# Kernel tuning notes

Measured on AMD Instinct MI355X. Metric: run time of the kernel, lower is better.

Reference implementation:

```python
import jax, jax.numpy as jnp
import numpy as np

N = 100000
D = 512   # input_size
C = 2     # output_class
QDIM = 128


def setup_inputs() -> dict:
    key = jax.random.key(0)
    ks = jax.random.split(key, 12)
    s = 0.02
    return {
        "feats": jax.random.normal(ks[0], (N, D), jnp.float32),
        "c": jax.random.normal(ks[1], (N, C), jnp.float32),
        "single_predictions": jax.random.normal(ks[2], (N, 1), jnp.float32),
        # self.lin = Linear(D, D) + ReLU
        "W_lin": jax.random.normal(ks[3], (D, D), jnp.float32) * s,
        "b_lin": jnp.zeros((D,), jnp.float32),
        # self.q = Linear(D, 128) + Tanh
        "W_q": jax.random.normal(ks[4], (QDIM, D), jnp.float32) * s,
        "b_q": jnp.zeros((QDIM,), jnp.float32),
        # self.v = Dropout(0.0) + Linear(D, D)
        "W_v": jax.random.normal(ks[5], (D, D), jnp.float32) * s,
        "b_v": jnp.zeros((D,), jnp.float32),
        # self.fcc = Conv1d(C, C, kernel_size=D)
        "W_fcc": jax.random.normal(ks[6], (C, C, D), jnp.float32) * s,
        "b_fcc": jnp.zeros((C,), jnp.float32),
    }


def reference(feats, c, single_predictions, W_lin, b_lin, W_q, b_q, W_v, b_v, W_fcc, b_fcc):
    n = feats.shape[0]
    k = int(0.2 * n)

    preds = single_predictions[:, 0]                      # [N]
    # torch.topk(largest=False): indices of the k smallest; zero them out
    _, lastk_idx = jax.lax.top_k(-preds, k)
    preds = preds.at[lastk_idx].set(0.0)
    instance_score = jax.nn.softmax(preds, axis=0)[:, None]  # [N,1], softmax over instances

    f = feats * instance_score + feats                    # [N,D]
    f = jax.nn.relu(f @ W_lin.T + b_lin)                  # self.lin
    V = f @ W_v.T + b_v                                   # [N,D] (dropout p=0)
    Q = jnp.tanh(f @ W_q.T + b_q)                         # [N,128]

    # torch.sort(c, 0, descending)[1][0,:] == per-class argmax over instances
    m_indices = jnp.argmax(c, axis=0)                     # [C]
    m_feats = f[m_indices]                                # [C,D]
    q_max = jnp.tanh(m_feats @ W_q.T + b_q)               # [C,128]

    A = Q @ q_max.T                                       # [N,C]
    A = jax.nn.softmax(A / jnp.sqrt(jnp.float32(QDIM)), axis=0)  # softmax over instances
    B = A.T @ V                                           # [C,D]

    # Conv1d(C, C, kernel=D) on B[None] -> length-1 output: full contraction
    Cout = jnp.einsum('id,oid->o', B, W_fcc) + b_fcc      # [C]
    return Cout[None, :], A, B
```

## Files before the change

kernel.cpp:

```cpp
#include <hip/hip_runtime.h>
#include <stdint.h>

typedef unsigned short u16;
typedef __bf16 bf16t;
typedef bf16t bf16x8 __attribute__((ext_vector_type(8)));
typedef float f32x4 __attribute__((ext_vector_type(4)));
typedef unsigned long long ull;

#define NROWS 100000
#define DD 512
#define QD 128
#define KSEL 20000
#define NB 1563

__device__ __forceinline__ uint32_t fmono(float x){
  uint32_t u = __float_as_uint(x);
  return (u & 0x80000000u) ? ~u : (u | 0x80000000u);
}
__device__ __forceinline__ float finv(uint32_t k){
  uint32_t u = (k & 0x80000000u) ? (k & 0x7fffffffu) : ~k;
  return __uint_as_float(u);
}
__device__ __forceinline__ u16 f2bf(float x){
  uint32_t u = __float_as_uint(x);
  u += 0x7fffu + ((u >> 16) & 1u);
  return (u16)(u >> 16);
}
__device__ __forceinline__ uint32_t pkbf(float a, float b){
  return (uint32_t)f2bf(a) | ((uint32_t)f2bf(b) << 16);
}

struct Scal {
  uint32_t keyT;
  float Z;
  uint32_t pad[14];
};

#define MFMA16(A,B,C) __builtin_amdgcn_mfma_f32_16x16x32_bf16(A,B,C,0,0,0)

__global__ void k_conv(const float* __restrict__ Wl, const float* __restrict__ Wv,
                       const float* __restrict__ Wq, u16* __restrict__ wl_bf, u16* __restrict__ wvq_bf,
                       uint32_t* __restrict__ hist, ull* __restrict__ cmax){
  int idx = blockIdx.x*256 + threadIdx.x;
  if (idx < 65536) hist[idx] = 0u;
  if (idx == 0){ cmax[0] = 0ull; cmax[1] = 0ull; }
  if (idx < 262144) wl_bf[idx] = f2bf(Wl[idx]);
  int e = idx - 262144;
  if (e >= 0) wvq_bf[e] = f2bf(e < 262144 ? Wv[e] : Wq[e - 262144]);
}

__global__ void k_sel1(const float* __restrict__ preds, const float* __restrict__ c,
                       uint32_t* __restrict__ hist, ull* __restrict__ cmax){
  __shared__ ull kr0[4], kr1[4];
  const int t = threadIdx.x;
  const int gid = blockIdx.x*256 + t;
  const int lane = t & 63;

  const float4* p4 = (const float4*)preds;
  for (int i = gid; i < 25000; i += 65536){
    float4 v = p4[i];
    atomicAdd(&hist[fmono(v.x) >> 16], 1u);
    atomicAdd(&hist[fmono(v.y) >> 16], 1u);
    atomicAdd(&hist[fmono(v.z) >> 16], 1u);
    atomicAdd(&hist[fmono(v.w) >> 16], 1u);
  }

  ull k0 = 0ull, k1 = 0ull;
  const float4* c4 = (const float4*)c;
  for (int i = gid; i < 50000; i += 65536){
    float4 v = c4[i];
    uint32_t r0 = 2u*i, r1 = 2u*i + 1u;
    ull a0 = ((ull)fmono(v.x) << 32) | (ull)(~r0);
    ull a1 = ((ull)fmono(v.z) << 32) | (ull)(~r1);
    ull b0 = ((ull)fmono(v.y) << 32) | (ull)(~r0);
    ull b1 = ((ull)fmono(v.w) << 32) | (ull)(~r1);
    if (a0 > k0) k0 = a0;
    if (a1 > k0) k0 = a1;
    if (b0 > k1) k1 = b0;
    if (b1 > k1) k1 = b1;
  }
  #pragma unroll
  for (int off = 32; off; off >>= 1){
    ull o0 = __shfl_xor(k0, off); if (o0 > k0) k0 = o0;
    ull o1 = __shfl_xor(k1, off); if (o1 > k1) k1 = o1;
  }
  if (lane == 0){ kr0[t >> 6] = k0; kr1[t >> 6] = k1; }
  __syncthreads();
  if (t == 0){
    ull m0 = kr0[0], m1 = kr1[0];
    #pragma unroll
    for (int w = 1; w < 4; ++w){
      if (kr0[w] > m0) m0 = kr0[w];
      if (kr1[w] > m1) m1 = kr1[w];
    }
    atomicMax(&cmax[0], m0);
    atomicMax(&cmax[1], m1);
  }
}

#define CAND_CAP 8192
__launch_bounds__(1024)
__global__ void k_prep2(const float* __restrict__ preds, const float* __restrict__ feats,
                        const float* __restrict__ Wl, const float* __restrict__ bl,
                        const float* __restrict__ Wq, const float* __restrict__ bq,
                        const uint32_t* __restrict__ hist, const ull* __restrict__ cmax,
                        Scal* __restrict__ sc, float* __restrict__ qmv){
  __shared__ uint32_t cand[CAND_CAP];
  __shared__ uint32_t wsum[16], woff[16];
  __shared__ float zred[16];
  __shared__ uint32_t s_B, s_cumBelow, s_keyT, candN;
  __shared__ float s_Z;
  __shared__ uint32_t s_mi[2];
  __shared__ float fmX[2][512];
  __shared__ float fmF[2][512];
  const int t = threadIdx.x;
  const int lane = t & 63, wv = t >> 6;

  if (t == 0){
    candN = 0;
    s_mi[0] = ~(uint32_t)(cmax[0] & 0xffffffffull);
    s_mi[1] = ~(uint32_t)(cmax[1] & 0xffffffffull);
  }

  const int b0 = t*64;
  uint32_t local = 0;
  {
    const uint4* h4 = (const uint4*)(hist + b0);
    #pragma unroll 4
    for (int q = 0; q < 16; ++q){ uint4 hv = h4[q]; local += hv.x + hv.y + hv.z + hv.w; }
  }
  uint32_t x = local;
  #pragma unroll
  for (int off = 1; off < 64; off <<= 1){
    uint32_t y = __shfl_up(x, off);
    if (lane >= off) x += y;
  }
  if (lane == 63) wsum[wv] = x;
  __syncthreads();
  if (t == 0){
    uint32_t cum = 0;
    for (int w = 0; w < 16; ++w){ woff[w] = cum; cum += wsum[w]; }
  }
  __syncthreads();
  uint32_t excl = x - local + woff[wv];
  if (excl < KSEL && excl + local >= KSEL){
    uint32_t cum = excl;
    for (int b = 0; b < 64; ++b){
      uint32_t h = hist[b0 + b];
      if (cum + h >= KSEL){ s_B = (uint32_t)(b0 + b); s_cumBelow = cum; break; }
      cum += h;
    }
  }
  __syncthreads();
  const uint32_t B = s_B;

  float sA = 0.f;
  const float4* p4 = (const float4*)preds;
  for (int i = t; i < 25000; i += 1024){
    float4 v = p4[i];
    float vv[4] = {v.x, v.y, v.z, v.w};
    #pragma unroll
    for (int e = 0; e < 4; ++e){
      uint32_t k = fmono(vv[e]);
      uint32_t bb = k >> 16;
      if (bb > B){
        sA += __expf(vv[e]);
      } else if (bb == B){
        uint32_t idx = atomicAdd(&candN, 1u);
        if (idx < CAND_CAP) cand[idx] = k;
      }
    }
  }
  #pragma unroll
  for (int off = 32; off; off >>= 1) sA += __shfl_xor(sA, off);
  if (lane == 0) zred[wv] = sA;
  __syncthreads();

  const uint32_t n = candN < CAND_CAP ? candN : CAND_CAP;
  const uint32_t r = KSEL - s_cumBelow;
  for (uint32_t i = t; i < n; i += 1024){
    uint32_t ki = cand[i];
    uint32_t less = 0, eq = 0;
    for (uint32_t j = 0; j < n; ++j){
      uint32_t kj = cand[j];
      less += (kj < ki) ? 1u : 0u;
      eq   += (kj == ki) ? 1u : 0u;
    }
    if (less < r && r <= less + eq) s_keyT = ki;
  }
  __syncthreads();
  const uint32_t keyT = s_keyT;

  float sCA = 0.f;
  for (uint32_t i = t; i < n; i += 1024){
    uint32_t k = cand[i];
    if (k > keyT) sCA += __expf(finv(k));
  }
  #pragma unroll
  for (int off = 32; off; off >>= 1) sCA += __shfl_xor(sCA, off);
  if (lane == 0) zred[wv] += sCA;
  __syncthreads();
  if (t == 0){
    float Z = (float)KSEL;
    for (int w = 0; w < 16; ++w) Z += zred[w];
    s_Z = Z;
    sc->keyT = keyT; sc->Z = Z;
  }
  __syncthreads();

  {
    int j = t >> 9, col = t & 511;
    fmX[j][col] = feats[(size_t)s_mi[j]*DD + col];
  }
  __syncthreads();

  {
    int nn = t >> 1, h = t & 1;
    const float4* wr4 = (const float4*)(Wl + (size_t)nn*DD + h*256);
    const float4* x04 = (const float4*)(&fmX[0][h*256]);
    const float4* x14 = (const float4*)(&fmX[1][h*256]);
    float a0 = 0.f, a1 = 0.f;
    #pragma unroll 4
    for (int k = 0; k < 64; ++k){
      float4 w = wr4[k], u = x04[k], v = x14[k];
      a0 += u.x*w.x + u.y*w.y + u.z*w.z + u.w*w.w;
      a1 += v.x*w.x + v.y*w.y + v.z*w.z + v.w*w.w;
    }
    a0 += __shfl_xor(a0, 1);
    a1 += __shfl_xor(a1, 1);
    if (h == 0){
      float Z = s_Z;
      float p0 = preds[s_mi[0]]; float q0 = (fmono(p0) <= keyT) ? 0.f : p0;
      float g0 = 1.f + __expf(q0) / Z;
      float p1 = preds[s_mi[1]]; float q1 = (fmono(p1) <= keyT) ? 0.f : p1;
      float g1 = 1.f + __expf(q1) / Z;
      float v0 = bl[nn] + g0*a0; fmF[0][nn] = v0 > 0.f ? v0 : 0.f;
      float v1 = bl[nn] + g1*a1; fmF[1][nn] = v1 > 0.f ? v1 : 0.f;
    }
  }
  __syncthreads();

  if (t < 256){
    int q = t & 127, j = t >> 7;
    const float4* wr4 = (const float4*)(Wq + (size_t)q*DD);
    const float4* x4  = (const float4*)(fmF[j]);
    float a0 = 0.f, a1 = 0.f;
    #pragma unroll 4
    for (int k = 0; k < 128; k += 2){
      float4 w0 = wr4[k], u0 = x4[k];
      float4 w1 = wr4[k+1], u1 = x4[k+1];
      a0 += u0.x*w0.x + u0.y*w0.y + u0.z*w0.z + u0.w*w0.w;
      a1 += u1.x*w1.x + u1.y*w1.y + u1.z*w1.z + u1.w*w1.w;
    }
    qmv[j*QD + q] = tanhf(bq[q] + a0 + a1);
  }
}

__device__ __forceinline__ const u16* chunk_src(const u16* __restrict__ wl,
                                                const u16* __restrict__ wvq,
                                                int ci, int r, int p){
  if (ci < 64){
    int nt = ci >> 4, kc = ci & 15;
    return wl + (size_t)(nt*128 + r)*DD + kc*32 + p*16;
  }
  int c2 = ci - 64;
  int nt2 = c2 >> 4, kc = c2 & 15;
  int colbase = (nt2 == 0) ? 512 : (nt2 - 1)*128;
  return wvq + (size_t)(colbase + r)*DD + kc*32 + p*16;
}

__launch_bounds__(256, 2)
__global__ void k_fused(const float* __restrict__ feats, const float* __restrict__ preds,
                        const u16* __restrict__ wl, const u16* __restrict__ wvq,
                        const float* __restrict__ bl, const float* __restrict__ bv,
                        const float* __restrict__ bq, const float* __restrict__ qmv,
                        const Scal* __restrict__ sc,
                        float* __restrict__ gpart, float* __restrict__ gpartE,
                        float* __restrict__ Aout){
  __shared__ __align__(16) u16 lds[38400];
  __shared__ __align__(16) float Ef[128];
  u16* AF = lds;
  u16* Wb = lds + 33280;
  float* sred = (float*)(lds + 33280);
  const int tid = threadIdx.x;
  const int lane = tid & 63, quad = lane >> 4, l16 = lane & 15;
  const int wave = tid >> 6, wm = wave >> 1, wn = wave & 1;
  const long i0 = (long)blockIdx.x * 64;
  const uint32_t keyT = sc->keyT;
  const float Z = sc->Z;

  {
    int row = lane;
    long ir = i0 + row; if (ir >= NROWS) ir = NROWS - 1;
    float p = preds[ir];
    float pm = (fmono(p) <= keyT) ? 0.f : p;
    float g = 1.f + __expf(pm) / Z;
    const float4* src = (const float4*)(feats + ir*DD + wave*128);
    u16* dst = AF + row*520 + wave*128;
    #pragma unroll
    for (int j = 0; j < 16; ++j){
      float4 a = src[2*j], b = src[2*j + 1];
      uint4 pk;
      pk.x = pkbf(a.x*g, a.y*g); pk.y = pkbf(a.z*g, a.w*g);
      pk.z = pkbf(b.x*g, b.y*g); pk.w = pkbf(b.z*g, b.w*g);
      *(uint4*)(dst + j*8) = pk;
    }
  }

  const int rS = tid >> 1, pS = tid & 1;
  u16* wdst = Wb + rS*40 + pS*16;
  uint4 w0, w1;
  { const u16* sp = chunk_src(wl, wvq, 0, rS, pS); w0 = *(const uint4*)sp; w1 = *(const uint4*)(sp + 8); }

  f32x4 acc[2][4];
  uint32_t pkF[4][16];
  int ci = 0;

  for (int nt = 0; nt < 4; ++nt){
    #pragma unroll
    for (int mi = 0; mi < 2; ++mi)
      #pragma unroll
      for (int ni = 0; ni < 4; ++ni) acc[mi][ni] = (f32x4){0.f,0.f,0.f,0.f};
    for (int kc = 0; kc < 16; ++kc, ++ci){
      __syncthreads();
      *(uint4*)wdst = w0; *(uint4*)(wdst + 8) = w1;
      __syncthreads();
      if (ci < 143){
        const u16* sp = chunk_src(wl, wvq, ci + 1, rS, pS);
        w0 = *(const uint4*)sp; w1 = *(const uint4*)(sp + 8);
      }
      bf16x8 a0 = *(const bf16x8*)&AF[(wm*32 + l16)*520 + kc*32 + quad*8];
      bf16x8 a1 = *(const bf16x8*)&AF[(wm*32 + 16 + l16)*520 + kc*32 + quad*8];
      bf16x8 b0 = *(const bf16x8*)&Wb[(wn*64 +  0 + l16)*40 + quad*8];
      bf16x8 b1 = *(const bf16x8*)&Wb[(wn*64 + 16 + l16)*40 + quad*8];
      bf16x8 b2 = *(const bf16x8*)&Wb[(wn*64 + 32 + l16)*40 + quad*8];
      bf16x8 b3 = *(const bf16x8*)&Wb[(wn*64 + 48 + l16)*40 + quad*8];
      acc[0][0] = MFMA16(a0, b0, acc[0][0]);
      acc[0][1] = MFMA16(a0, b1, acc[0][1]);
      acc[0][2] = MFMA16(a0, b2, acc[0][2]);
      acc[0][3] = MFMA16(a0, b3, acc[0][3]);
      acc[1][0] = MFMA16(a1, b0, acc[1][0]);
      acc[1][1] = MFMA16(a1, b1, acc[1][1]);
      acc[1][2] = MFMA16(a1, b2, acc[1][2]);
      acc[1][3] = MFMA16(a1, b3, acc[1][3]);
    }
    #pragma unroll
    for (int ni = 0; ni < 4; ++ni){
      float bb = bl[nt*128 + wn*64 + ni*16 + l16];
      #pragma unroll
      for (int mi = 0; mi < 2; ++mi){
        float e0 = acc[mi][ni][0] + bb; e0 = e0 > 0.f ? e0 : 0.f;
        float e1 = acc[mi][ni][1] + bb; e1 = e1 > 0.f ? e1 : 0.f;
        float e2 = acc[mi][ni][2] + bb; e2 = e2 > 0.f ? e2 : 0.f;
        float e3 = acc[mi][ni][3] + bb; e3 = e3 > 0.f ? e3 : 0.f;
        pkF[nt][mi*8 + ni*2 + 0] = pkbf(e0, e1);
        pkF[nt][mi*8 + ni*2 + 1] = pkbf(e2, e3);
      }
    }
  }

  __syncthreads();
  #pragma unroll
  for (int nt = 0; nt < 4; ++nt)
    #pragma unroll
    for (int ni = 0; ni < 4; ++ni)
      #pragma unroll
      for (int mi = 0; mi < 2; ++mi){
        int col = nt*128 + wn*64 + ni*16 + l16;
        int r0 = (wm*32 + mi*16 + quad*4)*520 + col;
        uint32_t x = pkF[nt][mi*8 + ni*2], y = pkF[nt][mi*8 + ni*2 + 1];
        AF[r0]        = (u16)x;
        AF[r0 + 520]  = (u16)(x >> 16);
        AF[r0 + 1040] = (u16)y;
        AF[r0 + 1560] = (u16)(y >> 16);
      }

  for (int nt2 = 0; nt2 < 5; ++nt2){
    #pragma unroll
    for (int mi = 0; mi < 2; ++mi)
      #pragma unroll
      for (int ni = 0; ni < 4; ++ni) acc[mi][ni] = (f32x4){0.f,0.f,0.f,0.f};
    for (int kc = 0; kc < 16; ++kc, ++ci){
      __syncthreads();
      *(uint4*)wdst = w0; *(uint4*)(wdst + 8) = w1;
      __syncthreads();
      if (ci < 143){
        const u16* sp = chunk_src(wl, wvq, ci + 1, rS, pS);
        w0 = *(const uint4*)sp; w1 = *(const uint4*)(sp + 8);
      }
      bf16x8 a0 = *(const bf16x8*)&AF[(wm*32 + l16)*520 + kc*32 + quad*8];
      bf16x8 a1 = *(const bf16x8*)&AF[(wm*32 + 16 + l16)*520 + kc*32 + quad*8];
      bf16x8 b0 = *(const bf16x8*)&Wb[(wn*64 +  0 + l16)*40 + quad*8];
      bf16x8 b1 = *(const bf16x8*)&Wb[(wn*64 + 16 + l16)*40 + quad*8];
      bf16x8 b2 = *(const bf16x8*)&Wb[(wn*64 + 32 + l16)*40 + quad*8];
      bf16x8 b3 = *(const bf16x8*)&Wb[(wn*64 + 48 + l16)*40 + quad*8];
      acc[0][0] = MFMA16(a0, b0, acc[0][0]);
      acc[0][1] = MFMA16(a0, b1, acc[0][1]);
      acc[0][2] = MFMA16(a0, b2, acc[0][2]);
      acc[0][3] = MFMA16(a0, b3, acc[0][3]);
      acc[1][0] = MFMA16(a1, b0, acc[1][0]);
      acc[1][1] = MFMA16(a1, b1, acc[1][1]);
      acc[1][2] = MFMA16(a1, b2, acc[1][2]);
      acc[1][3] = MFMA16(a1, b3, acc[1][3]);
    }
    if (nt2 == 0){
      float p0[2][4], p1[2][4];
      #pragma unroll
      for (int mi = 0; mi < 2; ++mi)
        #pragma unroll
        for (int e = 0; e < 4; ++e){ p0[mi][e] = 0.f; p1[mi][e] = 0.f; }
      #pragma unroll
      for (int ni = 0; ni < 4; ++ni){
        int qc = wn*64 + ni*16 + l16;
        float bqv = bq[qc], q0 = qmv[qc], q1 = qmv[QD + qc];
        #pragma unroll
        for (int mi = 0; mi < 2; ++mi)
          #pragma unroll
          for (int e = 0; e < 4; ++e){
            float tq = tanhf(acc[mi][ni][e] + bqv);
            p0[mi][e] += tq * q0;
            p1[mi][e] += tq * q1;
          }
      }
      #pragma unroll
      for (int off = 1; off <= 8; off <<= 1)
        #pragma unroll
        for (int mi = 0; mi < 2; ++mi)
          #pragma unroll
          for (int e = 0; e < 4; ++e){
            p0[mi][e] += __shfl_xor(p0[mi][e], off);
            p1[mi][e] += __shfl_xor(p1[mi][e], off);
          }
      __syncthreads();
      if (l16 == 0){
        #pragma unroll
        for (int mi = 0; mi < 2; ++mi)
          #pragma unroll
          for (int e = 0; e < 4; ++e){
            int row = wm*32 + mi*16 + quad*4 + e;
            sred[(row*2 + 0)*2 + wn] = p0[mi][e];
            sred[(row*2 + 1)*2 + wn] = p1[mi][e];
          }
      }
      __syncthreads();
      if (tid < 128){
        int row = tid >> 1, j = tid & 1;
        float sv = (sred[(row*2 + j)*2 + 0] + sred[(row*2 + j)*2 + 1]) * 0.08838834764831845f;
        bool valid = (i0 + row) < NROWS;
        float ev = valid ? __expf(sv) : 0.f;
        Ef[row*2 + j] = ev;
        if (valid) Aout[(i0 + row)*2 + j] = ev;
        float t2 = ev;
        #pragma unroll
        for (int off = 2; off <= 32; off <<= 1) t2 += __shfl_xor(t2, off);
        if (lane < 2) gpartE[(size_t)blockIdx.x*4 + (tid >> 6)*2 + j] = t2;
      }
      __syncthreads();
    } else {
      float e0[2][4], e1[2][4];
      #pragma unroll
      for (int mi = 0; mi < 2; ++mi)
        #pragma unroll
        for (int e = 0; e < 4; ++e){
          int row = wm*32 + mi*16 + quad*4 + e;
          e0[mi][e] = Ef[row*2 + 0];
          e1[mi][e] = Ef[row*2 + 1];
        }
      #pragma unroll
      for (int ni = 0; ni < 4; ++ni){
        int colv = (nt2 - 1)*128 + wn*64 + ni*16 + l16;
        float bvv = bv[colv];
        float b0 = 0.f, b1 = 0.f;
        #pragma unroll
        for (int mi = 0; mi < 2; ++mi)
          #pragma unroll
          for (int e = 0; e < 4; ++e){
            float v = acc[mi][ni][e] + bvv;
            b0 += v * e0[mi][e];
            b1 += v * e1[mi][e];
          }
        b0 += __shfl_xor(b0, 16); b0 += __shfl_xor(b0, 32);
        b1 += __shfl_xor(b1, 16); b1 += __shfl_xor(b1, 32);
        if (quad == 0){
          gpart[((size_t)blockIdx.x*2 + wm)*1024 + colv]       = b0;
          gpart[((size_t)blockIdx.x*2 + wm)*1024 + 512 + colv] = b1;
        }
      }
    }
  }
}

__global__ void k_red(const float* __restrict__ gpart, const float* __restrict__ gpartE,
                      float* __restrict__ sumEV, float* __restrict__ sumE){
  const int t = threadIdx.x;
  if (blockIdx.x == 256){
    __shared__ float r0[256], r1[256];
    float s0 = 0.f, s1 = 0.f;
    for (int i = t; i < NB*2; i += 256){ s0 += gpartE[(size_t)i*2]; s1 += gpartE[(size_t)i*2 + 1]; }
    r0[t] = s0; r1[t] = s1;
    __syncthreads();
    for (int st = 128; st; st >>= 1){
      if (t < st){ r0[t] += r0[t + st]; r1[t] += r1[t + st]; }
      __syncthreads();
    }
    if (t == 0){ sumE[0] = r0[0]; sumE[1] = r1[0]; }
    return;
  }
  __shared__ float4 red[256];
  int col4 = blockIdx.x * 4;
  float4 s = {0.f, 0.f, 0.f, 0.f};
  for (int r = t; r < NB*2; r += 256){
    float4 v = *(const float4*)(gpart + (size_t)r*1024 + col4);
    s.x += v.x; s.y += v.y; s.z += v.z; s.w += v.w;
  }
  red[t] = s;
  __syncthreads();
  for (int st = 128; st; st >>= 1){
    if (t < st){
      float4 o = red[t + st];
      red[t].x += o.x; red[t].y += o.y; red[t].z += o.z; red[t].w += o.w;
    }
    __syncthreads();
  }
  if (t == 0) *(float4*)(sumEV + col4) = red[0];
}

__global__ void k_post(float* __restrict__ out, const float* __restrict__ sumE,
                       const float* __restrict__ sumEV, const float* __restrict__ Wfcc,
                       const float* __restrict__ bfcc){
  if (blockIdx.x < 782){
    int idx = blockIdx.x*256 + threadIdx.x;
    if (idx < 200000) out[2 + idx] = out[2 + idx] / sumE[idx & 1];
    return;
  }
  __shared__ float red[512];
  int t = threadIdx.x;
  float z0 = sumE[0], z1 = sumE[1];
  float c0 = 0.f, c1 = 0.f;
  for (int e = t; e < 1024; e += 256){
    float bvv = sumEV[e] / ((e >> 9) ? z1 : z0);
    out[200002 + e] = bvv;
    c0 += bvv * Wfcc[e];
    c1 += bvv * Wfcc[1024 + e];
  }
  red[t] = c0; red[256 + t] = c1;
  __syncthreads();
  for (int s = 128; s; s >>= 1){
    if (t < s){ red[t] += red[t + s]; red[256 + t] += red[256 + t + s]; }
    __syncthreads();
  }
  if (t == 0){ out[0] = red[0] + bfcc[0]; out[1] = red[256] + bfcc[1]; }
}

extern "C" void kernel_launch(void* const* d_in, const int* in_sizes, int n_in,
                              void* d_out, int out_size, void* d_ws, size_t ws_size,
                              hipStream_t stream){
  (void)in_sizes; (void)n_in; (void)out_size; (void)ws_size;
  const float* feats = (const float*)d_in[0];
  const float* c     = (const float*)d_in[1];
  const float* preds = (const float*)d_in[2];
  const float* W_lin = (const float*)d_in[3];
  const float* b_lin = (const float*)d_in[4];
  const float* W_q   = (const float*)d_in[5];
  const float* b_q   = (const float*)d_in[6];
  const float* W_v   = (const float*)d_in[7];
  const float* b_v   = (const float*)d_in[8];
  const float* W_fcc = (const float*)d_in[9];
  const float* b_fcc = (const float*)d_in[10];
  float* out = (float*)d_out;
  char* ws = (char*)d_ws;

  u16*   wl_bf  = (u16*)(ws + 0);
  u16*   wvq_bf = (u16*)(ws + 524288);
  Scal*  sc     = (Scal*)(ws + 1179648);
  float* qmv    = (float*)(ws + 1179712);
  float* sumE   = (float*)(ws + 1180736);
  float* sumEV  = (float*)(ws + 1180800);
  float* gpartE = (float*)(ws + 1184896);
  float* gpart  = (float*)(ws + 1209984);
  uint32_t* hist = (uint32_t*)(ws + 1209984);
  ull*      cmax = (ull*)(ws + 1209984 + 262144);

  k_conv <<<2304, 256, 0, stream>>>(W_lin, W_v, W_q, wl_bf, wvq_bf, hist, cmax);
  k_sel1 <<<256, 256, 0, stream>>>(preds, c, hist, cmax);
  k_prep2<<<1, 1024, 0, stream>>>(preds, feats, W_lin, b_lin, W_q, b_q, hist, cmax, sc, qmv);
  k_fused<<<NB, 256, 0, stream>>>(feats, preds, wl_bf, wvq_bf, b_lin, b_v, b_q,
                                  qmv, sc, gpart, gpartE, out + 2);
  k_red  <<<257, 256, 0, stream>>>(gpart, gpartE, sumEV, sumE);
  k_post <<<783, 256, 0, stream>>>(out, sumE, sumEV, W_fcc, b_fcc);
}
```

Baseline: 732.3 us.

## Double-buffer weight chunks in LDS with XOR swizzle and pre-tiled weight layout

The weight conversion kernel now writes bf16 weights already tiled into contiguous 128x32 chunks in the order the fused kernel consumes them, so each thread does one contiguous 32-byte load per chunk. The fused kernel switches from a single LDS weight buffer with two barriers per k-step to ping-pong buffers with one barrier per step and a two-chunk-deep register prefetch. Padded LDS rows are replaced by XOR-swizzled layouts to avoid bank conflicts. The exp weights are also kept in registers instead of an LDS array. The intent is to hide global load latency and halve barrier cost in the MFMA loop, at the price of more complex indexing and extra registers.

```diff
diff --git a/kernel.cpp b/kernel.cpp
--- a/kernel.cpp
+++ b/kernel.cpp
@@ -39,14 +39,26 @@
 #define MFMA16(A,B,C) __builtin_amdgcn_mfma_f32_16x16x32_bf16(A,B,C,0,0,0)
 
 __global__ void k_conv(const float* __restrict__ Wl, const float* __restrict__ Wv,
-                       const float* __restrict__ Wq, u16* __restrict__ wl_bf, u16* __restrict__ wvq_bf,
+                       const float* __restrict__ Wq, u16* __restrict__ wch,
                        uint32_t* __restrict__ hist, ull* __restrict__ cmax){
   int idx = blockIdx.x*256 + threadIdx.x;
   if (idx < 65536) hist[idx] = 0u;
   if (idx == 0){ cmax[0] = 0ull; cmax[1] = 0ull; }
-  if (idx < 262144) wl_bf[idx] = f2bf(Wl[idx]);
-  int e = idx - 262144;
-  if (e >= 0) wvq_bf[e] = f2bf(e < 262144 ? Wv[e] : Wq[e - 262144]);
+  int ci  = idx >> 12;
+  int rem = idx & 4095;
+  int r   = rem >> 5;
+  int col = rem & 31;
+  float v;
+  if (ci < 64){
+    int nt = ci >> 4, kc = ci & 15;
+    v = Wl[(size_t)(nt*128 + r)*DD + kc*32 + col];
+  } else {
+    int c2 = ci - 64;
+    int nt2 = c2 >> 4, kc = c2 & 15;
+    if (nt2 == 0) v = Wq[(size_t)r*DD + kc*32 + col];
+    else          v = Wv[(size_t)((nt2-1)*128 + r)*DD + kc*32 + col];
+  }
+  wch[idx] = f2bf(v);
 }
 
 __global__ void k_sel1(const float* __restrict__ preds, const float* __restrict__ c,
@@ -256,32 +268,19 @@
   }
 }
 
-__device__ __forceinline__ const u16* chunk_src(const u16* __restrict__ wl,
-                                                const u16* __restrict__ wvq,
-                                                int ci, int r, int p){
-  if (ci < 64){
-    int nt = ci >> 4, kc = ci & 15;
-    return wl + (size_t)(nt*128 + r)*DD + kc*32 + p*16;
-  }
-  int c2 = ci - 64;
-  int nt2 = c2 >> 4, kc = c2 & 15;
-  int colbase = (nt2 == 0) ? 512 : (nt2 - 1)*128;
-  return wvq + (size_t)(colbase + r)*DD + kc*32 + p*16;
-}
-
 __launch_bounds__(256, 2)
 __global__ void k_fused(const float* __restrict__ feats, const float* __restrict__ preds,
-                        const u16* __restrict__ wl, const u16* __restrict__ wvq,
+                        const u16* __restrict__ wch,
                         const float* __restrict__ bl, const float* __restrict__ bv,
                         const float* __restrict__ bq, const float* __restrict__ qmv,
                         const Scal* __restrict__ sc,
                         float* __restrict__ gpart, float* __restrict__ gpartE,
                         float* __restrict__ Aout){
-  __shared__ __align__(16) u16 lds[38400];
-  __shared__ __align__(16) float Ef[128];
-  u16* AF = lds;
-  u16* Wb = lds + 33280;
-  float* sred = (float*)(lds + 33280);
+  __shared__ __align__(16) u16 lds[40960];
+  u16* AF  = lds;
+  u16* WB0 = lds + 32768;
+  u16* WB1 = lds + 36864;
+  float* sred = (float*)WB1;
   const int tid = threadIdx.x;
   const int lane = tid & 63, quad = lane >> 4, l16 = lane & 15;
   const int wave = tid >> 6, wm = wave >> 1, wn = wave & 1;
@@ -296,53 +295,82 @@
     float pm = (fmono(p) <= keyT) ? 0.f : p;
     float g = 1.f + __expf(pm) / Z;
     const float4* src = (const float4*)(feats + ir*DD + wave*128);
-    u16* dst = AF + row*520 + wave*128;
+    u16* dstrow = AF + row*512;
+    const int swz = row & 7;
     #pragma unroll
     for (int j = 0; j < 16; ++j){
       float4 a = src[2*j], b = src[2*j + 1];
       uint4 pk;
       pk.x = pkbf(a.x*g, a.y*g); pk.y = pkbf(a.z*g, a.w*g);
       pk.z = pkbf(b.x*g, b.y*g); pk.w = pkbf(b.z*g, b.w*g);
-      *(uint4*)(dst + j*8) = pk;
-    }
-  }
-
+      int blk = (wave << 4) | j;
+      *(uint4*)&dstrow[(blk ^ swz) << 3] = pk;
+    }
+  }
+
+  const u16* wsrc = wch + (size_t)tid * 16;
   const int rS = tid >> 1, pS = tid & 1;
-  u16* wdst = Wb + rS*40 + pS*16;
-  uint4 w0, w1;
-  { const u16* sp = chunk_src(wl, wvq, 0, rS, pS); w0 = *(const uint4*)sp; w1 = *(const uint4*)(sp + 8); }
+  const int offA = rS*32 + ((((pS << 1)    ) ^ (rS & 3)) << 3);
+  const int offB = rS*32 + ((((pS << 1) | 1) ^ (rS & 3)) << 3);
+  uint4 pA0 = *(const uint4*)(wsrc);
+  uint4 pA1 = *(const uint4*)(wsrc + 8);
+  uint4 pB0 = *(const uint4*)(wsrc + 4096);
+  uint4 pB1 = *(const uint4*)(wsrc + 4096 + 8);
+  *(uint4*)&WB0[offA] = pA0;
+  *(uint4*)&WB0[offB] = pA1;
+  pA0 = *(const uint4*)(wsrc + 8192);
+  pA1 = *(const uint4*)(wsrc + 8192 + 8);
+  __syncthreads();
+
+  const int sb  = l16 & 7;
+  const int sb2 = l16 & 3;
+  const int base_a = (wm*32 + l16) * 512;
+  const int rB = wn*64 + l16;
+  const int qsw = (quad ^ sb2) << 3;
+  const int off_b0 = (rB +  0)*32 + qsw;
+  const int off_b1 = (rB + 16)*32 + qsw;
+  const int off_b2 = (rB + 32)*32 + qsw;
+  const int off_b3 = (rB + 48)*32 + qsw;
 
   f32x4 acc[2][4];
   uint32_t pkF[4][16];
+  float eR0[2][4], eR1[2][4];
   int ci = 0;
+
+#define KSTEP(BUFC, BUFN, P0, P1)                                                  \
+  {                                                                                \
+    int abk = (((ci & 15) << 2) | quad) ^ sb;                                      \
+    bf16x8 a0 = *(const bf16x8*)&AF[base_a + (abk << 3)];                          \
+    bf16x8 a1 = *(const bf16x8*)&AF[base_a + 8192 + (abk << 3)];                   \
+    bf16x8 b0 = *(const bf16x8*)&BUFC[off_b0];                                     \
+    bf16x8 b1 = *(const bf16x8*)&BUFC[off_b1];                                     \
+    bf16x8 b2 = *(const bf16x8*)&BUFC[off_b2];                                     \
+    bf16x8 b3 = *(const bf16x8*)&BUFC[off_b3];                                     \
+    if (ci + 1 < 144){ *(uint4*)&BUFN[offA] = P0; *(uint4*)&BUFN[offB] = P1; }     \
+    if (ci + 3 < 144){                                                             \
+      const u16* s_ = wsrc + (size_t)(ci + 3)*4096;                                \
+      P0 = *(const uint4*)s_; P1 = *(const uint4*)(s_ + 8);                        \
+    }                                                                              \
+    acc[0][0] = MFMA16(a0, b0, acc[0][0]);                                         \
+    acc[0][1] = MFMA16(a0, b1, acc[0][1]);                                         \
+    acc[0][2] = MFMA16(a0, b2, acc[0][2]);                                         \
+    acc[0][3] = MFMA16(a0, b3, acc[0][3]);                                         \
+    acc[1][0] = MFMA16(a1, b0, acc[1][0]);                                         \
+    acc[1][1] = MFMA16(a1, b1, acc[1][1]);                                         \
+    acc[1][2] = MFMA16(a1, b2, acc[1][2]);                                         \
+    acc[1][3] = MFMA16(a1, b3, acc[1][3]);                                         \
+    __syncthreads();                                                               \
+    ++ci;                                                                          \
+  }
 
   for (int nt = 0; nt < 4; ++nt){
     #pragma unroll
     for (int mi = 0; mi < 2; ++mi)
       #pragma unroll
       for (int ni = 0; ni < 4; ++ni) acc[mi][ni] = (f32x4){0.f,0.f,0.f,0.f};
-    for (int kc = 0; kc < 16; ++kc, ++ci){
-      __syncthreads();
-      *(uint4*)wdst = w0; *(uint4*)(wdst + 8) = w1;
-      __syncthreads();
-      if (ci < 143){
-        const u16* sp = chunk_src(wl, wvq, ci + 1, rS, pS);
-        w0 = *(const uint4*)sp; w1 = *(const uint4*)(sp + 8);
-      }
-      bf16x8 a0 = *(const bf16x8*)&AF[(wm*32 + l16)*520 + kc*32 + quad*8];
-      bf16x8 a1 = *(const bf16x8*)&AF[(wm*32 + 16 + l16)*520 + kc*32 + quad*8];
-      bf16x8 b0 = *(const bf16x8*)&Wb[(wn*64 +  0 + l16)*40 + quad*8];
-      bf16x8 b1 = *(const bf16x8*)&Wb[(wn*64 + 16 + l16)*40 + quad*8];
-      bf16x8 b2 = *(const bf16x8*)&Wb[(wn*64 + 32 + l16)*40 + quad*8];
-      bf16x8 b3 = *(const bf16x8*)&Wb[(wn*64 + 48 + l16)*40 + quad*8];
-      acc[0][0] = MFMA16(a0, b0, acc[0][0]);
-      acc[0][1] = MFMA16(a0, b1, acc[0][1]);
-      acc[0][2] = MFMA16(a0, b2, acc[0][2]);
-      acc[0][3] = MFMA16(a0, b3, acc[0][3]);
-      acc[1][0] = MFMA16(a1, b0, acc[1][0]);
-      acc[1][1] = MFMA16(a1, b1, acc[1][1]);
-      acc[1][2] = MFMA16(a1, b2, acc[1][2]);
-      acc[1][3] = MFMA16(a1, b3, acc[1][3]);
+    for (int kh = 0; kh < 8; ++kh){
+      KSTEP(WB0, WB1, pB0, pB1);
+      KSTEP(WB1, WB0, pA0, pA1);
     }
     #pragma unroll
     for (int ni = 0; ni < 4; ++ni){
@@ -359,7 +387,6 @@
     }
   }
 
-  __syncthreads();
   #pragma unroll
   for (int nt = 0; nt < 4; ++nt)
     #pragma unroll
@@ -367,41 +394,24 @@
       #pragma unroll
       for (int mi = 0; mi < 2; ++mi){
         int col = nt*128 + wn*64 + ni*16 + l16;
-        int r0 = (wm*32 + mi*16 + quad*4)*520 + col;
+        int r0 = wm*32 + mi*16 + quad*4;
         uint32_t x = pkF[nt][mi*8 + ni*2], y = pkF[nt][mi*8 + ni*2 + 1];
-        AF[r0]        = (u16)x;
-        AF[r0 + 520]  = (u16)(x >> 16);
-        AF[r0 + 1040] = (u16)y;
-        AF[r0 + 1560] = (u16)(y >> 16);
+        int cb = col >> 3, cw = col & 7;
+        AF[(r0+0)*512 + (((cb) ^ ((r0+0)&7)) << 3) + cw] = (u16)x;
+        AF[(r0+1)*512 + (((cb) ^ ((r0+1)&7)) << 3) + cw] = (u16)(x >> 16);
+        AF[(r0+2)*512 + (((cb) ^ ((r0+2)&7)) << 3) + cw] = (u16)y;
+        AF[(r0+3)*512 + (((cb) ^ ((r0+3)&7)) << 3) + cw] = (u16)(y >> 16);
       }
+  __syncthreads();
 
   for (int nt2 = 0; nt2 < 5; ++nt2){
     #pragma unroll
     for (int mi = 0; mi < 2; ++mi)
       #pragma unroll
       for (int ni = 0; ni < 4; ++ni) acc[mi][ni] = (f32x4){0.f,0.f,0.f,0.f};
-    for (int kc = 0; kc < 16; ++kc, ++ci){
-      __syncthreads();
-      *(uint4*)wdst = w0; *(uint4*)(wdst + 8) = w1;
-      __syncthreads();
-      if (ci < 143){
-        const u16* sp = chunk_src(wl, wvq, ci + 1, rS, pS);
-        w0 = *(const uint4*)sp; w1 = *(const uint4*)(sp + 8);
-      }
-      bf16x8 a0 = *(const bf16x8*)&AF[(wm*32 + l16)*520 + kc*32 + quad*8];
-      bf16x8 a1 = *(const bf16x8*)&AF[(wm*32 + 16 + l16)*520 + kc*32 + quad*8];
-      bf16x8 b0 = *(const bf16x8*)&Wb[(wn*64 +  0 + l16)*40 + quad*8];
-      bf16x8 b1 = *(const bf16x8*)&Wb[(wn*64 + 16 + l16)*40 + quad*8];
-      bf16x8 b2 = *(const bf16x8*)&Wb[(wn*64 + 32 + l16)*40 + quad*8];
-      bf16x8 b3 = *(const bf16x8*)&Wb[(wn*64 + 48 + l16)*40 + quad*8];
-      acc[0][0] = MFMA16(a0, b0, acc[0][0]);
-      acc[0][1] = MFMA16(a0, b1, acc[0][1]);
-      acc[0][2] = MFMA16(a0, b2, acc[0][2]);
-      acc[0][3] = MFMA16(a0, b3, acc[0][3]);
-      acc[1][0] = MFMA16(a1, b0, acc[1][0]);
-      acc[1][1] = MFMA16(a1, b1, acc[1][1]);
-      acc[1][2] = MFMA16(a1, b2, acc[1][2]);
-      acc[1][3] = MFMA16(a1, b3, acc[1][3]);
+    for (int kh = 0; kh < 8; ++kh){
+      KSTEP(WB0, WB1, pB0, pB1);
+      KSTEP(WB1, WB0, pA0, pA1);
     }
     if (nt2 == 0){
       float p0[2][4], p1[2][4];
@@ -431,7 +441,6 @@
             p0[mi][e] += __shfl_xor(p0[mi][e], off);
             p1[mi][e] += __shfl_xor(p1[mi][e], off);
           }
-      __syncthreads();
       if (l16 == 0){
         #pragma unroll
         for (int mi = 0; mi < 2; ++mi)
@@ -443,12 +452,22 @@
           }
       }
       __syncthreads();
+      #pragma unroll
+      for (int mi = 0; mi < 2; ++mi)
+        #pragma unroll
+        for (int e = 0; e < 4; ++e){
+          int row = wm*32 + mi*16 + quad*4 + e;
+          bool valid = (i0 + row) < NROWS;
+          float sv0 = (sred[(row*2 + 0)*2 + 0] + sred[(row*2 + 0)*2 + 1]) * 0.08838834764831845f;
+          float sv1 = (sred[(row*2 + 1)*2 + 0] + sred[(row*2 + 1)*2 + 1]) * 0.08838834764831845f;
+          eR0[mi][e] = valid ? __expf(sv0) : 0.f;
+          eR1[mi][e] = valid ? __expf(sv1) : 0.f;
+        }
       if (tid < 128){
         int row = tid >> 1, j = tid & 1;
         float sv = (sred[(row*2 + j)*2 + 0] + sred[(row*2 + j)*2 + 1]) * 0.08838834764831845f;
         bool valid = (i0 + row) < NROWS;
         float ev = valid ? __expf(sv) : 0.f;
-        Ef[row*2 + j] = ev;
         if (valid) Aout[(i0 + row)*2 + j] = ev;
         float t2 = ev;
         #pragma unroll
@@ -457,15 +476,6 @@
       }
       __syncthreads();
     } else {
-      float e0[2][4], e1[2][4];
-      #pragma unroll
-      for (int mi = 0; mi < 2; ++mi)
-        #pragma unroll
-        for (int e = 0; e < 4; ++e){
-          int row = wm*32 + mi*16 + quad*4 + e;
-          e0[mi][e] = Ef[row*2 + 0];
-          e1[mi][e] = Ef[row*2 + 1];
-        }
       #pragma unroll
       for (int ni = 0; ni < 4; ++ni){
         int colv = (nt2 - 1)*128 + wn*64 + ni*16 + l16;
@@ -476,8 +486,8 @@
           #pragma unroll
           for (int e = 0; e < 4; ++e){
             float v = acc[mi][ni][e] + bvv;
-            b0 += v * e0[mi][e];
-            b1 += v * e1[mi][e];
+            b0 += v * eR0[mi][e];
+            b1 += v * eR1[mi][e];
           }
         b0 += __shfl_xor(b0, 16); b0 += __shfl_xor(b0, 32);
         b1 += __shfl_xor(b1, 16); b1 += __shfl_xor(b1, 32);
@@ -488,6 +498,7 @@
       }
     }
   }
+#undef KSTEP
 }
 
 __global__ void k_red(const float* __restrict__ gpart, const float* __restrict__ gpartE,
@@ -570,8 +581,7 @@
   float* out = (float*)d_out;
   char* ws = (char*)d_ws;
 
-  u16*   wl_bf  = (u16*)(ws + 0);
-  u16*   wvq_bf = (u16*)(ws + 524288);
+  u16*   wch    = (u16*)(ws + 0);
   Scal*  sc     = (Scal*)(ws + 1179648);
   float* qmv    = (float*)(ws + 1179712);
   float* sumE   = (float*)(ws + 1180736);
@@ -581,10 +591,10 @@
   uint32_t* hist = (uint32_t*)(ws + 1209984);
   ull*      cmax = (ull*)(ws + 1209984 + 262144);
 
-  k_conv <<<2304, 256, 0, stream>>>(W_lin, W_v, W_q, wl_bf, wvq_bf, hist, cmax);
+  k_conv <<<2304, 256, 0, stream>>>(W_lin, W_v, W_q, wch, hist, cmax);
   k_sel1 <<<256, 256, 0, stream>>>(preds, c, hist, cmax);
   k_prep2<<<1, 1024, 0, stream>>>(preds, feats, W_lin, b_lin, W_q, b_q, hist, cmax, sc, qmv);
-  k_fused<<<NB, 256, 0, stream>>>(feats, preds, wl_bf, wvq_bf, b_lin, b_v, b_q,
+  k_fused<<<NB, 256, 0, stream>>>(feats, preds, wch, b_lin, b_v, b_q,
                                   qmv, sc, gpart, gpartE, out + 2);
   k_red  <<<257, 256, 0, stream>>>(gpart, gpartE, sumEV, sumE);
   k_post <<<783, 256, 0, stream>>>(out, sumE, sumEV, W_fcc, b_fcc);
```

New measurement: 633.0 us. -13.6%, faster.
